# Kernel tuning notes

Measured on AMD Instinct MI355X. Metric: run time of the kernel, lower is better.

## Reference

```python
import jax, jax.numpy as jnp
import numpy as np

N_NODES = 50000
N_EDGES = 1600000
DIM_IN = 64
DIM = 64
DIM_OUT = 32
N_GRAPHS = 64
DELTA = 2.5749
BN_EPS = 1e-5


def _lin(x, W, b):
    return x @ W.T + b


def _pna_conv(x, src, dst, mlp_W, mlp_b, W1, b1, W2, b2):
    # GINConv with overridden PNA aggregate: nn(x + aggr(x_j))
    msgs = x[src]                                               # [E, d]
    n = x.shape[0]
    sums = jax.ops.segment_sum(msgs, dst, num_segments=n)       # [N, d]
    maxs = jax.ops.segment_max(msgs, dst, num_segments=n)
    cnt = jax.ops.segment_sum(jnp.ones((msgs.shape[0], 1), msgs.dtype), dst,
                              num_segments=n)                   # [N, 1]
    means = sums / cnt
    var = jax.nn.relu(jax.ops.segment_sum(msgs * msgs, dst, num_segments=n) / cnt
                      - means * means)
    aggr = jnp.concatenate([sums, maxs, means, var], axis=1)    # [N, 4d]
    comb = jnp.concatenate([aggr, (cnt / DELTA) * aggr, (DELTA / cnt) * aggr],
                           axis=1)                              # [N, 12d]
    a = _lin(comb, mlp_W, mlp_b)                                # [N, d]
    h = x + a                                                   # (1+eps)*x + aggr, eps=0
    return _lin(jax.nn.relu(_lin(h, W1, b1)), W2, b2)


def _bn(x, g, b):
    # BatchNorm1d with batch statistics (training-mode stats, biased var)
    m = x.mean(axis=0)
    v = ((x - m) ** 2).mean(axis=0)
    return g * (x - m) / jnp.sqrt(v + BN_EPS) + b


def setup_inputs() -> dict:
    key = jax.random.key(0)
    ks = jax.random.split(key, 32)
    x = jax.random.normal(ks[0], (N_NODES, DIM_IN), dtype=jnp.float32)
    src = jax.random.randint(ks[1], (N_EDGES,), 0, N_NODES)
    dst = jax.random.randint(ks[2], (N_EDGES,), 0, N_NODES)
    # guarantee every node has >=1 incoming edge (original divides by bincount)
    dst = dst.at[:N_NODES].set(jnp.arange(N_NODES))
    edge_index = jnp.stack([src, dst]).astype(jnp.int32)
    batch = jnp.sort(jax.random.randint(ks[3], (N_NODES,), 0, N_GRAPHS)).astype(jnp.int32)

    def w(k, shape):
        return jax.random.normal(k, shape, dtype=jnp.float32) * 0.1

    d = {"x": x, "edge_index": edge_index, "batch": batch}
    i = 4
    for c in ("c1", "c2", "c3"):
        d[f"{c}_mlp_W"] = w(ks[i], (DIM, DIM * 12)); i += 1
        d[f"{c}_mlp_b"] = jnp.zeros((DIM,), jnp.float32)
        d[f"{c}_W1"] = w(ks[i], (DIM, DIM)); i += 1
        d[f"{c}_b1"] = jnp.zeros((DIM,), jnp.float32)
        d[f"{c}_W2"] = w(ks[i], (DIM, DIM)); i += 1
        d[f"{c}_b2"] = jnp.zeros((DIM,), jnp.float32)
    for b in ("bn1", "bn2", "bn3"):
        d[f"{b}_g"] = jnp.ones((DIM,), jnp.float32)
        d[f"{b}_b"] = jnp.zeros((DIM,), jnp.float32)
    d["fc1_W"] = w(ks[i], (DIM, DIM)); i += 1
    d["fc1_b"] = jnp.zeros((DIM,), jnp.float32)
    d["fc2_W"] = w(ks[i], (DIM_OUT, DIM)); i += 1
    d["fc2_b"] = jnp.zeros((DIM_OUT,), jnp.float32)
    return d


def reference(x, edge_index, batch,
              c1_mlp_W, c1_mlp_b, c1_W1, c1_b1, c1_W2, c1_b2, bn1_g, bn1_b,
              c2_mlp_W, c2_mlp_b, c2_W1, c2_b1, c2_W2, c2_b2, bn2_g, bn2_b,
              c3_mlp_W, c3_mlp_b, c3_W1, c3_b1, c3_W2, c3_b2, bn3_g, bn3_b,
              fc1_W, fc1_b, fc2_W, fc2_b):
    src, dst = edge_index[0], edge_index[1]
    h = jax.nn.relu(_pna_conv(x, src, dst, c1_mlp_W, c1_mlp_b, c1_W1, c1_b1, c1_W2, c1_b2))
    h = _bn(h, bn1_g, bn1_b)
    h = jax.nn.relu(_pna_conv(h, src, dst, c2_mlp_W, c2_mlp_b, c2_W1, c2_b1, c2_W2, c2_b2))
    h = _bn(h, bn2_g, bn2_b)
    h = jax.nn.relu(_pna_conv(h, src, dst, c3_mlp_W, c3_mlp_b, c3_W1, c3_b1, c3_W2, c3_b2))
    h = _bn(h, bn3_g, bn3_b)
    g = jax.ops.segment_sum(h, batch, num_segments=N_GRAPHS)   # global_add_pool
    g = jax.nn.relu(_lin(g, fc1_W, fc1_b))                     # dropout disabled (eval)
    g = _lin(g, fc2_W, fc2_b)
    return jax.nn.log_softmax(g, axis=-1)
```

## Files before the change

kernel.cpp:

```cpp
#include <hip/hip_runtime.h>

#define NN 50000
#define NE 1600000
#define DD 64
#define NGRAPH 64
#define DOUT 32
#define DELTA_F 2.5749f
#define BN_EPS_F 1e-5f

typedef unsigned short ushort;
typedef __attribute__((ext_vector_type(8))) short short8;
typedef __attribute__((ext_vector_type(4))) float floatx4;

static __device__ __forceinline__ float blo(unsigned u) {
    return __uint_as_float(u << 16);
}
static __device__ __forceinline__ float bhi(unsigned u) {
    return __uint_as_float(u & 0xFFFF0000u);
}
static __device__ __forceinline__ float bu2f(ushort u) {
    return __uint_as_float(((unsigned)u) << 16);
}
static __device__ __forceinline__ ushort f2bu(float f) {
    unsigned u = __float_as_uint(f);
    unsigned r = (u + 0x7FFF + ((u >> 16) & 1)) >> 16;
    return (ushort)r;
}
static __device__ __forceinline__ unsigned pk(float a, float b) {
    return ((unsigned)f2bu(b) << 16) | (unsigned)f2bu(a);
}

__global__ void k_init(int* __restrict__ counts, float* __restrict__ bnstat,
                       float* __restrict__ gpool) {
    int i = blockIdx.x * 256 + threadIdx.x;
    if (i < NN) counts[i] = 0;
    if (i < 384) bnstat[i] = 0.f;
    if (i < NGRAPH * DD) gpool[i] = 0.f;
}

__global__ void k_rank(const int* __restrict__ dst, int* __restrict__ counts,
                       int* __restrict__ rank) {
    int e = blockIdx.x * 256 + threadIdx.x;
    if (e < NE) rank[e] = atomicAdd(&counts[dst[e]], 1);
}

__global__ void k_scan_a(const int* __restrict__ counts, int* __restrict__ blockSums) {
    __shared__ int red[256];
    int tid = threadIdx.x;
    int gid = blockIdx.x * 256 + tid;
    int v = (gid < NN) ? counts[gid] : 0;
    red[tid] = v;
    __syncthreads();
    for (int s = 128; s > 0; s >>= 1) {
        if (tid < s) red[tid] += red[tid + s];
        __syncthreads();
    }
    if (tid == 0) blockSums[blockIdx.x] = red[0];
}

__global__ void k_scan_b(const int* __restrict__ blockSums, int* __restrict__ blockBase) {
    __shared__ int sh[256];
    int tid = threadIdx.x;
    int v = (tid < 196) ? blockSums[tid] : 0;
    sh[tid] = v;
    __syncthreads();
    for (int off = 1; off < 256; off <<= 1) {
        int t = (tid >= off) ? sh[tid - off] : 0;
        __syncthreads();
        sh[tid] += t;
        __syncthreads();
    }
    blockBase[tid] = sh[tid] - v;
}

__global__ void k_scan_c(const int* __restrict__ counts, const int* __restrict__ blockBase,
                         int* __restrict__ row_ptr) {
    __shared__ int sh[256];
    int tid = threadIdx.x;
    int gid = blockIdx.x * 256 + tid;
    int v = (gid < NN) ? counts[gid] : 0;
    sh[tid] = v;
    __syncthreads();
    for (int off = 1; off < 256; off <<= 1) {
        int t = (tid >= off) ? sh[tid - off] : 0;
        __syncthreads();
        sh[tid] += t;
        __syncthreads();
    }
    int excl = blockBase[blockIdx.x] + sh[tid] - v;
    if (gid <= NN) row_ptr[gid] = excl;
}

__global__ void k_place(const int* __restrict__ src, const int* __restrict__ dst,
                        const int* __restrict__ rank, const int* __restrict__ row_ptr,
                        int* __restrict__ csr_src) {
    int e = blockIdx.x * 256 + threadIdx.x;
    if (e < NE) csr_src[row_ptr[dst[e]] + rank[e]] = src[e];
}

__global__ void k_wprep(const float* __restrict__ w0, const float* __restrict__ w1,
                        const float* __restrict__ w2,
                        const float* __restrict__ a0, const float* __restrict__ a1,
                        const float* __restrict__ a2, const float* __restrict__ a3,
                        const float* __restrict__ a4, const float* __restrict__ a5,
                        ushort* __restrict__ Wb, float* __restrict__ Wsm) {
    int i = blockIdx.x * 256 + threadIdx.x;
    if (i < 3 * 65536) {
        int layer = i / 65536, r = i % 65536;
        const float* w = (layer == 0) ? w0 : ((layer == 1) ? w1 : w2);
        int c = r / 16384, r2 = r % 16384;
        int kb = r2 >> 11, r3 = r2 & 2047;
        int t = r3 >> 9, r4 = r3 & 511;
        int l = r4 >> 3, j = r4 & 7;
        int k = kb * 32 + (l >> 4) * 8 + j;
        int o = t * 16 + (l & 15);
        int g = (c == 0) ? 0 : ((c == 3) ? 2 : 1);
        float wv = w[o * 768 + g * 256 + k];
        ushort h = f2bu(wv);
        Wb[i] = (c == 2) ? f2bu(wv - bu2f(h)) : h;
    } else if (i < 3 * 65536 + 6 * 4096) {
        int r2 = i - 3 * 65536;
        int l = r2 >> 12, r = r2 & 4095;
        const float* w = (l == 0) ? a0 : (l == 1) ? a1 : (l == 2) ? a2
                       : (l == 3) ? a3 : (l == 4) ? a4 : a5;
        int o = r >> 6, j = r & 63;
        Wsm[l * 4096 + j * 64 + o] = w[r];
    }
}

__global__ void k_x2h(const float* __restrict__ x, ushort* __restrict__ XH) {
    int i = blockIdx.x * 256 + threadIdx.x;
    if (i < NN * 16) {
        float4 v = *(const float4*)(x + (size_t)i * 4);
        ushort4 h;
        h.x = f2bu(v.x); h.y = f2bu(v.y); h.z = f2bu(v.z); h.w = f2bu(v.w);
        *(ushort4*)(XH + (size_t)i * 4) = h;
    }
}

#define MBIAS(i) aux[i]
#define B1V(i)   aux[64 + (i)]
#define B2V(i)   aux[128 + (i)]
#define DEGV(m)  aux[192 + (m)]

__global__ __launch_bounds__(256, 4) void k_fused(
    const ushort* __restrict__ XH,
    const int* __restrict__ row_ptr, const int* __restrict__ csr_src,
    const ushort* __restrict__ Wbh,
    const float* __restrict__ mlp_b,
    const float* __restrict__ W1t, const float* __restrict__ b1,
    const float* __restrict__ W2t, const float* __restrict__ b2,
    float* __restrict__ Y, float* __restrict__ bnstat) {
    __shared__ __align__(16) char smem[26624];
    ushort* const Agh = (ushort*)smem;
    ushort* const Agl = (ushort*)(smem + 12800);
    float* const aux = (float*)(smem + 25600);
    float* const hsf = (float*)smem;

    const int tid = threadIdx.x;
    const int node0 = blockIdx.x * 32;

    if (tid < 64) {
        MBIAS(tid) = mlp_b[tid];
        B1V(tid) = b1[tid];
        B2V(tid) = b2[tid];
    }

    {
        const int l8 = tid & 7;
        const int m = tid >> 3;
        const int node = node0 + m;
        const int f0 = l8 * 8;
        const ushort* Xp = XH + f0;

        float s[8], q[8], mx[8];
#pragma unroll
        for (int i = 0; i < 8; ++i) { s[i] = 0.f; q[i] = 0.f; mx[i] = -3.402823466e38f; }

        auto acc8 = [&](const uint4& rr) {
            float v0 = blo(rr.x), v1 = bhi(rr.x);
            float v2 = blo(rr.y), v3 = bhi(rr.y);
            float v4 = blo(rr.z), v5 = bhi(rr.z);
            float v6 = blo(rr.w), v7 = bhi(rr.w);
            s[0] += v0; q[0] = fmaf(v0, v0, q[0]); mx[0] = fmaxf(mx[0], v0);
            s[1] += v1; q[1] = fmaf(v1, v1, q[1]); mx[1] = fmaxf(mx[1], v1);
            s[2] += v2; q[2] = fmaf(v2, v2, q[2]); mx[2] = fmaxf(mx[2], v2);
            s[3] += v3; q[3] = fmaf(v3, v3, q[3]); mx[3] = fmaxf(mx[3], v3);
            s[4] += v4; q[4] = fmaf(v4, v4, q[4]); mx[4] = fmaxf(mx[4], v4);
            s[5] += v5; q[5] = fmaf(v5, v5, q[5]); mx[5] = fmaxf(mx[5], v5);
            s[6] += v6; q[6] = fmaf(v6, v6, q[6]); mx[6] = fmaxf(mx[6], v6);
            s[7] += v7; q[7] = fmaf(v7, v7, q[7]); mx[7] = fmaxf(mx[7], v7);
        };

        int beg = 0, end = 0;
        if (node < NN) { beg = row_ptr[node]; end = row_ptr[node + 1]; }
        const int deg = end - beg;
        const int nb = (deg + 3) >> 2;

        uint4 ra[4], rb[4];
        int ia[4];
        if (nb > 0) {
#pragma unroll
            for (int j = 0; j < 4; ++j) {
                int e = beg + j;
                ia[j] = csr_src[(e < end) ? e : end - 1];
            }
#pragma unroll
            for (int j = 0; j < 4; ++j)
                ra[j] = *(const uint4*)(Xp + (size_t)ia[j] * 64);
            if (nb > 1) {
#pragma unroll
                for (int j = 0; j < 4; ++j) {
                    int e = beg + 4 + j;
                    ia[j] = csr_src[(e < end) ? e : end - 1];
                }
            }
        }
        for (int t = 0; t < nb; ++t) {
            if (t + 1 < nb) {
#pragma unroll
                for (int j = 0; j < 4; ++j)
                    rb[j] = *(const uint4*)(Xp + (size_t)ia[j] * 64);
            }
            if (t + 2 < nb) {
                int b2e = beg + (t + 2) * 4;
#pragma unroll
                for (int j = 0; j < 4; ++j) {
                    int e = b2e + j;
                    ia[j] = csr_src[(e < end) ? e : end - 1];
                }
            }
            int cnt = end - (beg + t * 4);
            if (cnt >= 4) {
#pragma unroll
                for (int j = 0; j < 4; ++j) acc8(ra[j]);
            } else {
#pragma unroll
                for (int j = 0; j < 4; ++j) if (j < cnt) acc8(ra[j]);
            }
            if (t + 1 < nb) {
#pragma unroll
                for (int j = 0; j < 4; ++j) ra[j] = rb[j];
            }
        }

        float cdeg = (node < NN) ? (float)deg : 1.f;
        float rc = 1.0f / cdeg;
        float var[8];
#pragma unroll
        for (int i = 0; i < 8; ++i) {
            float mean = s[i] * rc;
            var[i] = fmaxf(q[i] * rc - mean * mean, 0.f);
            if (node >= NN) { mx[i] = 0.f; var[i] = 0.f; }
        }
        ushort* dh = Agh + m * 200 + f0;
        ushort* dl = Agl + m * 200 + f0;
        auto emit8 = [&](const float* v, int off) {
            ushort h0 = f2bu(v[0]), h1 = f2bu(v[1]), h2 = f2bu(v[2]), h3 = f2bu(v[3]);
            ushort h4 = f2bu(v[4]), h5 = f2bu(v[5]), h6 = f2bu(v[6]), h7 = f2bu(v[7]);
            uint4 hv;
            hv.x = (unsigned)h0 | ((unsigned)h1 << 16);
            hv.y = (unsigned)h2 | ((unsigned)h3 << 16);
            hv.z = (unsigned)h4 | ((unsigned)h5 << 16);
            hv.w = (unsigned)h6 | ((unsigned)h7 << 16);
            uint4 lv;
            lv.x = pk(v[0] - bu2f(h0), v[1] - bu2f(h1));
            lv.y = pk(v[2] - bu2f(h2), v[3] - bu2f(h3));
            lv.z = pk(v[4] - bu2f(h4), v[5] - bu2f(h5));
            lv.w = pk(v[6] - bu2f(h6), v[7] - bu2f(h7));
            *(uint4*)(dh + off) = hv;
            *(uint4*)(dl + off) = lv;
        };
        emit8(s, 0);
        emit8(mx, 64);
        emit8(var, 128);
        if (l8 == 0) DEGV(m) = cdeg;
    }
    __syncthreads();

    const int ln = tid & 63, wvi = tid >> 6;
    const int quad = ln >> 4, l16 = ln & 15;
    const int mtile = wvi >> 1;
    const int nt0 = (wvi & 1) * 2;

    const ushort* ArowH = Agh + (mtile * 16 + l16) * 200 + quad * 8;
    const ushort* ArowL = Agl + (mtile * 16 + l16) * 200 + quad * 8;
    short8 afh[6], afl[6];
#pragma unroll
    for (int i = 0; i < 6; ++i) {
        const int off = (i >> 1) * 64 + (i & 1) * 32;
        afh[i] = *(const short8*)(ArowH + off);
        afl[i] = *(const short8*)(ArowL + off);
    }
    __syncthreads();

#pragma unroll
    for (int nti = 0; nti < 2; ++nti) {
        const int nt = nt0 + nti;
        floatx4 aA0 = (floatx4){0.f, 0.f, 0.f, 0.f};
        floatx4 aB0 = (floatx4){0.f, 0.f, 0.f, 0.f};
        floatx4 aA1 = (floatx4){0.f, 0.f, 0.f, 0.f};
        floatx4 aB1 = (floatx4){0.f, 0.f, 0.f, 0.f};
        floatx4 aA2 = (floatx4){0.f, 0.f, 0.f, 0.f};
        floatx4 aB2 = (floatx4){0.f, 0.f, 0.f, 0.f};
#pragma unroll
        for (int kb = 0; kb < 8; ++kb) {
            const int am = (kb < 4) ? kb : ((kb < 6) ? (kb - 4) : (kb - 2));
            const int base = ((kb * 4 + nt) * 512) + ln * 8;
            short8 w0 = *(const short8*)(Wbh + base);
            short8 w1h = *(const short8*)(Wbh + 16384 + base);
            short8 w2 = *(const short8*)(Wbh + 3 * 16384 + base);
            if (kb == 4 || kb == 5) {
                aB0 = __builtin_amdgcn_mfma_f32_16x16x32_bf16(afh[am], w0, aB0, 0, 0, 0);
                aB1 = __builtin_amdgcn_mfma_f32_16x16x32_bf16(afh[am], w1h, aB1, 0, 0, 0);
                aB2 = __builtin_amdgcn_mfma_f32_16x16x32_bf16(afh[am], w2, aB2, 0, 0, 0);
            } else {
                short8 w1l = *(const short8*)(Wbh + 2 * 16384 + base);
                aA0 = __builtin_amdgcn_mfma_f32_16x16x32_bf16(afh[am], w0, aA0, 0, 0, 0);
                aA1 = __builtin_amdgcn_mfma_f32_16x16x32_bf16(afh[am], w1h, aA1, 0, 0, 0);
                aA1 = __builtin_amdgcn_mfma_f32_16x16x32_bf16(afl[am], w1h, aA1, 0, 0, 0);
                aA1 = __builtin_amdgcn_mfma_f32_16x16x32_bf16(afh[am], w1l, aA1, 0, 0, 0);
                aA2 = __builtin_amdgcn_mfma_f32_16x16x32_bf16(afh[am], w2, aA2, 0, 0, 0);
            }
        }
#pragma unroll
        for (int r = 0; r < 4; ++r) {
            int m = mtile * 16 + quad * 4 + r;
            float dg = DEGV(m), rcd = 1.f / dg;
            float cA2 = DELTA_F * rcd;
            float cB2 = DELTA_F * rcd * rcd;
            float cA1 = dg * (1.0f / DELTA_F);
            int n = nt * 16 + l16;
            hsf[n * 34 + m] = aA0[r] + rcd * aB0[r]
                            + cA2 * aA2[r] + cB2 * aB2[r]
                            + cA1 * aA1[r] + (1.0f / DELTA_F) * aB1[r];
        }
    }
    __syncthreads();

    const int tx = tid & 15, ty = tid >> 4;
    const int o0 = tx * 4, n0 = ty * 2;
#pragma unroll
    for (int ni = 0; ni < 2; ++ni) {
        int n = n0 + ni;
        int node = node0 + n;
        float xa4[4] = {0.f, 0.f, 0.f, 0.f};
        if (node < NN) {
            ushort4 hx = *(const ushort4*)(XH + (size_t)node * DD + o0);
            xa4[0] = bu2f(hx.x); xa4[1] = bu2f(hx.y);
            xa4[2] = bu2f(hx.z); xa4[3] = bu2f(hx.w);
        }
#pragma unroll
        for (int oi = 0; oi < 4; ++oi) {
            int idx = (o0 + oi) * 34 + n;
            hsf[idx] = hsf[idx] + xa4[oi] + MBIAS(o0 + oi);
        }
    }
    __syncthreads();

    const float2* const hs2 = (const float2*)hsf;
    float l1[8];
#pragma unroll
    for (int i = 0; i < 8; ++i) l1[i] = 0.f;
#pragma unroll 4
    for (int j = 0; j < 64; ++j) {
        float2 a = hs2[j * 17 + ty];
        const float4 wv4 = *(const float4*)(W1t + j * 64 + o0);
        l1[0] += a.x * wv4.x; l1[1] += a.x * wv4.y; l1[2] += a.x * wv4.z; l1[3] += a.x * wv4.w;
        l1[4] += a.y * wv4.x; l1[5] += a.y * wv4.y; l1[6] += a.y * wv4.z; l1[7] += a.y * wv4.w;
    }
    __syncthreads();
#pragma unroll
    for (int ni = 0; ni < 2; ++ni)
#pragma unroll
        for (int oi = 0; oi < 4; ++oi)
            hsf[(o0 + oi) * 34 + n0 + ni] = fmaxf(l1[ni * 4 + oi] + B1V(o0 + oi), 0.f);
    __syncthreads();

    float l2[8];
#pragma unroll
    for (int i = 0; i < 8; ++i) l2[i] = 0.f;
#pragma unroll 4
    for (int j = 0; j < 64; ++j) {
        float2 a = hs2[j * 17 + ty];
        const float4 wv4 = *(const float4*)(W2t + j * 64 + o0);
        l2[0] += a.x * wv4.x; l2[1] += a.x * wv4.y; l2[2] += a.x * wv4.z; l2[3] += a.x * wv4.w;
        l2[4] += a.y * wv4.x; l2[5] += a.y * wv4.y; l2[6] += a.y * wv4.z; l2[7] += a.y * wv4.w;
    }
    __syncthreads();
#pragma unroll
    for (int ni = 0; ni < 2; ++ni) {
        int node = node0 + n0 + ni;
        float4 yv;
        yv.x = fmaxf(l2[ni * 4 + 0] + B2V(o0 + 0), 0.f);
        yv.y = fmaxf(l2[ni * 4 + 1] + B2V(o0 + 1), 0.f);
        yv.z = fmaxf(l2[ni * 4 + 2] + B2V(o0 + 2), 0.f);
        yv.w = fmaxf(l2[ni * 4 + 3] + B2V(o0 + 3), 0.f);
        if (node < NN) *(float4*)(Y + (size_t)node * DD + o0) = yv;
        hsf[(o0 + 0) * 34 + n0 + ni] = yv.x;
        hsf[(o0 + 1) * 34 + n0 + ni] = yv.y;
        hsf[(o0 + 2) * 34 + n0 + ni] = yv.z;
        hsf[(o0 + 3) * 34 + n0 + ni] = yv.w;
    }
    __syncthreads();

    if (tid < 64) {
        float s = 0.f, sq = 0.f;
        int lim = NN - node0;
        if (lim > 32) lim = 32;
        for (int n = 0; n < lim; ++n) {
            float v = hsf[tid * 34 + n];
            s += v;
            sq += v * v;
        }
        atomicAdd(&bnstat[tid], s);
        atomicAdd(&bnstat[64 + tid], sq);
    }
}

__global__ __launch_bounds__(256) void k_bnapply(
    const float* __restrict__ Y, const float* __restrict__ bs,
    const float* __restrict__ g, const float* __restrict__ b,
    ushort* __restrict__ XH,
    const int* __restrict__ batch, float* __restrict__ gpool, int do_pool) {
    __shared__ float sc[64], shf[64], pool[512];
    int tid = threadIdx.x;
    if (tid < 64) {
        float mean = bs[tid] * (1.f / NN);
        float var = fmaxf(bs[64 + tid] * (1.f / NN) - mean * mean, 0.f);
        float inv = rsqrtf(var + BN_EPS_F);
        float s = g[tid] * inv;
        sc[tid] = s;
        shf[tid] = b[tid] - mean * s;
    }
    __syncthreads();
    int i = blockIdx.x * 256 + tid;
    int n = i >> 4, fq = (i & 15) * 4;
    float4 r = make_float4(0.f, 0.f, 0.f, 0.f);
    bool valid = i < NN * 16;
    if (valid) {
        float4 y = *(const float4*)(Y + (size_t)i * 4);
        r.x = y.x * sc[fq + 0] + shf[fq + 0];
        r.y = y.y * sc[fq + 1] + shf[fq + 1];
        r.z = y.z * sc[fq + 2] + shf[fq + 2];
        r.w = y.w * sc[fq + 3] + shf[fq + 3];
        ushort4 h;
        h.x = f2bu(r.x); h.y = f2bu(r.y); h.z = f2bu(r.z); h.w = f2bu(r.w);
        *(ushort4*)(XH + (size_t)i * 4) = h;
    }
    if (do_pool) {
        int nfirst = blockIdx.x * 16;
        int nlast = nfirst + 15;
        if (nlast >= NN) nlast = NN - 1;
        int gmin = batch[nfirst], gmax = batch[nlast];
        int span = gmax - gmin + 1;
        if (span <= 8) {
            for (int j = tid; j < span * 64; j += 256) pool[j] = 0.f;
            __syncthreads();
            if (valid) {
                int gb = batch[n] - gmin;
                atomicAdd(&pool[gb * 64 + fq + 0], r.x);
                atomicAdd(&pool[gb * 64 + fq + 1], r.y);
                atomicAdd(&pool[gb * 64 + fq + 2], r.z);
                atomicAdd(&pool[gb * 64 + fq + 3], r.w);
            }
            __syncthreads();
            for (int j = tid; j < span * 64; j += 256)
                atomicAdd(&gpool[(size_t)(gmin + (j >> 6)) * 64 + (j & 63)], pool[j]);
        } else {
            if (valid) {
                float* gp = gpool + (size_t)batch[n] * DD + fq;
                atomicAdd(gp + 0, r.x);
                atomicAdd(gp + 1, r.y);
                atomicAdd(gp + 2, r.z);
                atomicAdd(gp + 3, r.w);
            }
        }
    }
}

__global__ __launch_bounds__(256) void k_head(const float* __restrict__ gpool,
                                              const float* __restrict__ fc1W, const float* __restrict__ fc1b,
                                              const float* __restrict__ fc2W, const float* __restrict__ fc2b,
                                              float* __restrict__ out) {
    __shared__ float sh[12576];
    float* const gs = sh;
    float* const w1t = sh + 4096;
    float* const z1s = sh + 8256;
    float* const b1s = sh + 12416;
    float* const b2s = sh + 12480;
    float* const w2t = sh;
    float* const z2s = sh + 4096;

    int tid = threadIdx.x;
    for (int i = tid; i < 4096; i += 256) {
        gs[i] = gpool[i];
        int o = i >> 6, j = i & 63;
        w1t[j * 65 + o] = fc1W[i];
    }
    if (tid < 64) b1s[tid] = fc1b[tid];
    if (tid < 32) b2s[tid] = fc2b[tid];
    __syncthreads();
    {
        int tx = tid & 15, ty = tid >> 4, o0 = tx * 4, g0 = ty * 4;
        float acc[16];
#pragma unroll
        for (int i = 0; i < 16; ++i) acc[i] = 0.f;
        for (int j = 0; j < 64; ++j) {
            float w0 = w1t[j * 65 + o0 + 0], w1 = w1t[j * 65 + o0 + 1];
            float w2 = w1t[j * 65 + o0 + 2], w3 = w1t[j * 65 + o0 + 3];
#pragma unroll
            for (int gi = 0; gi < 4; ++gi) {
                float a = gs[(g0 + gi) * 64 + j];
                acc[gi * 4 + 0] += a * w0; acc[gi * 4 + 1] += a * w1;
                acc[gi * 4 + 2] += a * w2; acc[gi * 4 + 3] += a * w3;
            }
        }
        __syncthreads();
#pragma unroll
        for (int gi = 0; gi < 4; ++gi)
#pragma unroll
            for (int oi = 0; oi < 4; ++oi)
                z1s[(g0 + gi) * 65 + o0 + oi] = fmaxf(acc[gi * 4 + oi] + b1s[o0 + oi], 0.f);
    }
    for (int i = tid; i < 2048; i += 256) {
        int o = i >> 6, j = i & 63;
        w2t[j * 33 + o] = fc2W[i];
    }
    __syncthreads();
    {
        int tx = tid & 7, ty = tid >> 3, o0 = tx * 4, g0 = ty * 2;
        float acc[8];
#pragma unroll
        for (int i = 0; i < 8; ++i) acc[i] = 0.f;
        for (int j = 0; j < 64; ++j) {
            float w0 = w2t[j * 33 + o0 + 0], w1 = w2t[j * 33 + o0 + 1];
            float w2 = w2t[j * 33 + o0 + 2], w3 = w2t[j * 33 + o0 + 3];
            float a0 = z1s[(g0 + 0) * 65 + j];
            float a1 = z1s[(g0 + 1) * 65 + j];
            acc[0] += a0 * w0; acc[1] += a0 * w1; acc[2] += a0 * w2; acc[3] += a0 * w3;
            acc[4] += a1 * w0; acc[5] += a1 * w1; acc[6] += a1 * w2; acc[7] += a1 * w3;
        }
#pragma unroll
        for (int gi = 0; gi < 2; ++gi)
#pragma unroll
            for (int oi = 0; oi < 4; ++oi)
                z2s[(g0 + gi) * 33 + o0 + oi] = acc[gi * 4 + oi] + b2s[o0 + oi];
    }
    __syncthreads();
    if (tid < 64) {
        float m = -3.402823466e38f;
        for (int c = 0; c < DOUT; ++c) m = fmaxf(m, z2s[tid * 33 + c]);
        float s = 0.f;
        for (int c = 0; c < DOUT; ++c) s += expf(z2s[tid * 33 + c] - m);
        float lse = m + logf(s);
        for (int c = 0; c < DOUT; ++c)
            out[tid * DOUT + c] = z2s[tid * 33 + c] - lse;
    }
}

extern "C" void kernel_launch(void* const* d_in, const int* in_sizes, int n_in,
                              void* d_out, int out_size, void* d_ws, size_t ws_size,
                              hipStream_t stream) {
    const float* x = (const float*)d_in[0];
    const int* ei = (const int*)d_in[1];
    const int* src = ei;
    const int* dst = ei + NE;
    const int* batch = (const int*)d_in[2];
    const float *mlpW[3], *mlpB[3], *w1[3], *bb1[3], *w2[3], *bb2[3], *bng[3], *bnb[3];
    for (int l = 0; l < 3; ++l) {
        mlpW[l] = (const float*)d_in[3 + 6 * l];
        mlpB[l] = (const float*)d_in[4 + 6 * l];
        w1[l]   = (const float*)d_in[5 + 6 * l];
        bb1[l]  = (const float*)d_in[6 + 6 * l];
        w2[l]   = (const float*)d_in[7 + 6 * l];
        bb2[l]  = (const float*)d_in[8 + 6 * l];
        bng[l]  = (const float*)d_in[21 + 2 * l];
        bnb[l]  = (const float*)d_in[22 + 2 * l];
    }
    const float* fc1W = (const float*)d_in[27];
    const float* fc1b = (const float*)d_in[28];
    const float* fc2W = (const float*)d_in[29];
    const float* fc2b = (const float*)d_in[30];
    float* out = (float*)d_out;

    char* ws = (char*)d_ws;
    size_t off = 0;
    auto alloc = [&](size_t bytes) -> void* {
        void* p = ws + off;
        off = (off + bytes + 511) & ~(size_t)511;
        return p;
    };
    int* counts    = (int*)alloc((size_t)NN * 4);
    int* row_ptr   = (int*)alloc((size_t)(NN + 1) * 4);
    int* rank      = (int*)alloc((size_t)NE * 4);
    int* blockSums = (int*)alloc(256 * 4);
    int* blockBase = (int*)alloc(256 * 4);
    int* csr_src   = (int*)alloc((size_t)NE * 4);
    float* Yb      = (float*)alloc((size_t)NN * DD * 4);
    ushort* XH     = (ushort*)alloc((size_t)NN * DD * 2);
    ushort* Wb     = (ushort*)alloc((size_t)3 * 65536 * 2);
    float* Wsm     = (float*)alloc((size_t)6 * 4096 * 4);
    float* bnstat  = (float*)alloc(384 * 4);
    float* gpool   = (float*)alloc((size_t)NGRAPH * DD * 4);
    (void)ws_size; (void)in_sizes; (void)n_in; (void)out_size;

    k_init<<<196, 256, 0, stream>>>(counts, bnstat, gpool);
    k_rank<<<6250, 256, 0, stream>>>(dst, counts, rank);
    k_scan_a<<<196, 256, 0, stream>>>(counts, blockSums);
    k_scan_b<<<1, 256, 0, stream>>>(blockSums, blockBase);
    k_scan_c<<<196, 256, 0, stream>>>(counts, blockBase, row_ptr);
    k_place<<<6250, 256, 0, stream>>>(src, dst, rank, row_ptr, csr_src);
    k_wprep<<<864, 256, 0, stream>>>(mlpW[0], mlpW[1], mlpW[2],
                                     w1[0], w2[0], w1[1], w2[1], w1[2], w2[2],
                                     Wb, Wsm);
    k_x2h<<<3125, 256, 0, stream>>>(x, XH);

    for (int l = 0; l < 3; ++l) {
        k_fused<<<1563, 256, 0, stream>>>(XH, row_ptr, csr_src,
                                          Wb + (size_t)l * 65536,
                                          mlpB[l],
                                          Wsm + (size_t)(2 * l) * 4096, bb1[l],
                                          Wsm + (size_t)(2 * l + 1) * 4096, bb2[l],
                                          Yb, bnstat + l * 128);
        k_bnapply<<<3125, 256, 0, stream>>>(Yb, bnstat + l * 128, bng[l], bnb[l],
                                            XH, batch, gpool, (l == 2) ? 1 : 0);
    }
    k_head<<<1, 256, 0, stream>>>(gpool, fc1W, fc1b, fc2W, fc2b, out);
}
```

Measured before the change: 523.9 us.

## Fold BatchNorm affine into next layer's aggregation and merge prep kernels

The per-layer BN-apply kernels are removed. Each layer now writes the pre-BN ReLU output straight to bf16, and the next fused kernel applies the BN affine algebraically to the aggregated sum, max, variance and the self term. The init, weight-prep and x-to-bf16 kernels are merged into one prep kernel, and only the final layer keeps an fp32 output for pooling. This cuts several launches and a full read/write pass over node features per layer. The cost is that BN is applied after bf16 rounding of the pre-BN values, which slightly changes numerics, and the max rewrite is only valid when the BN scale is non-negative.

```diff
diff --git a/kernel.cpp b/kernel.cpp
--- a/kernel.cpp
+++ b/kernel.cpp
@@ -30,81 +30,25 @@
     return ((unsigned)f2bu(b) << 16) | (unsigned)f2bu(a);
 }
 
-__global__ void k_init(int* __restrict__ counts, float* __restrict__ bnstat,
+__global__ void k_prep(const float* __restrict__ x, ushort* __restrict__ XH,
+                       const float* __restrict__ w0, const float* __restrict__ w1,
+                       const float* __restrict__ w2,
+                       const float* __restrict__ a0, const float* __restrict__ a1,
+                       const float* __restrict__ a2, const float* __restrict__ a3,
+                       const float* __restrict__ a4, const float* __restrict__ a5,
+                       ushort* __restrict__ Wb, float* __restrict__ Wsm,
+                       int* __restrict__ counts, float* __restrict__ bnstat,
                        float* __restrict__ gpool) {
     int i = blockIdx.x * 256 + threadIdx.x;
     if (i < NN) counts[i] = 0;
     if (i < 384) bnstat[i] = 0.f;
     if (i < NGRAPH * DD) gpool[i] = 0.f;
-}
-
-__global__ void k_rank(const int* __restrict__ dst, int* __restrict__ counts,
-                       int* __restrict__ rank) {
-    int e = blockIdx.x * 256 + threadIdx.x;
-    if (e < NE) rank[e] = atomicAdd(&counts[dst[e]], 1);
-}
-
-__global__ void k_scan_a(const int* __restrict__ counts, int* __restrict__ blockSums) {
-    __shared__ int red[256];
-    int tid = threadIdx.x;
-    int gid = blockIdx.x * 256 + tid;
-    int v = (gid < NN) ? counts[gid] : 0;
-    red[tid] = v;
-    __syncthreads();
-    for (int s = 128; s > 0; s >>= 1) {
-        if (tid < s) red[tid] += red[tid + s];
-        __syncthreads();
-    }
-    if (tid == 0) blockSums[blockIdx.x] = red[0];
-}
-
-__global__ void k_scan_b(const int* __restrict__ blockSums, int* __restrict__ blockBase) {
-    __shared__ int sh[256];
-    int tid = threadIdx.x;
-    int v = (tid < 196) ? blockSums[tid] : 0;
-    sh[tid] = v;
-    __syncthreads();
-    for (int off = 1; off < 256; off <<= 1) {
-        int t = (tid >= off) ? sh[tid - off] : 0;
-        __syncthreads();
-        sh[tid] += t;
-        __syncthreads();
-    }
-    blockBase[tid] = sh[tid] - v;
-}
-
-__global__ void k_scan_c(const int* __restrict__ counts, const int* __restrict__ blockBase,
-                         int* __restrict__ row_ptr) {
-    __shared__ int sh[256];
-    int tid = threadIdx.x;
-    int gid = blockIdx.x * 256 + tid;
-    int v = (gid < NN) ? counts[gid] : 0;
-    sh[tid] = v;
-    __syncthreads();
-    for (int off = 1; off < 256; off <<= 1) {
-        int t = (tid >= off) ? sh[tid - off] : 0;
-        __syncthreads();
-        sh[tid] += t;
-        __syncthreads();
-    }
-    int excl = blockBase[blockIdx.x] + sh[tid] - v;
-    if (gid <= NN) row_ptr[gid] = excl;
-}
-
-__global__ void k_place(const int* __restrict__ src, const int* __restrict__ dst,
-                        const int* __restrict__ rank, const int* __restrict__ row_ptr,
-                        int* __restrict__ csr_src) {
-    int e = blockIdx.x * 256 + threadIdx.x;
-    if (e < NE) csr_src[row_ptr[dst[e]] + rank[e]] = src[e];
-}
-
-__global__ void k_wprep(const float* __restrict__ w0, const float* __restrict__ w1,
-                        const float* __restrict__ w2,
-                        const float* __restrict__ a0, const float* __restrict__ a1,
-                        const float* __restrict__ a2, const float* __restrict__ a3,
-                        const float* __restrict__ a4, const float* __restrict__ a5,
-                        ushort* __restrict__ Wb, float* __restrict__ Wsm) {
-    int i = blockIdx.x * 256 + threadIdx.x;
+    if (i < NN * 16) {
+        float4 v = *(const float4*)(x + (size_t)i * 4);
+        ushort4 h;
+        h.x = f2bu(v.x); h.y = f2bu(v.y); h.z = f2bu(v.z); h.w = f2bu(v.w);
+        *(ushort4*)(XH + (size_t)i * 4) = h;
+    }
     if (i < 3 * 65536) {
         int layer = i / 65536, r = i % 65536;
         const float* w = (layer == 0) ? w0 : ((layer == 1) ? w1 : w2);
@@ -128,30 +72,85 @@
     }
 }
 
-__global__ void k_x2h(const float* __restrict__ x, ushort* __restrict__ XH) {
-    int i = blockIdx.x * 256 + threadIdx.x;
-    if (i < NN * 16) {
-        float4 v = *(const float4*)(x + (size_t)i * 4);
-        ushort4 h;
-        h.x = f2bu(v.x); h.y = f2bu(v.y); h.z = f2bu(v.z); h.w = f2bu(v.w);
-        *(ushort4*)(XH + (size_t)i * 4) = h;
-    }
+__global__ void k_rank(const int* __restrict__ dst, int* __restrict__ counts,
+                       int* __restrict__ rank) {
+    int e = blockIdx.x * 256 + threadIdx.x;
+    if (e < NE) rank[e] = atomicAdd(&counts[dst[e]], 1);
+}
+
+__global__ void k_scan_a(const int* __restrict__ counts, int* __restrict__ blockSums) {
+    __shared__ int red[256];
+    int tid = threadIdx.x;
+    int gid = blockIdx.x * 256 + tid;
+    int v = (gid < NN) ? counts[gid] : 0;
+    red[tid] = v;
+    __syncthreads();
+    for (int s = 128; s > 0; s >>= 1) {
+        if (tid < s) red[tid] += red[tid + s];
+        __syncthreads();
+    }
+    if (tid == 0) blockSums[blockIdx.x] = red[0];
+}
+
+__global__ void k_scan_b(const int* __restrict__ blockSums, int* __restrict__ blockBase) {
+    __shared__ int sh[256];
+    int tid = threadIdx.x;
+    int v = (tid < 196) ? blockSums[tid] : 0;
+    sh[tid] = v;
+    __syncthreads();
+    for (int off = 1; off < 256; off <<= 1) {
+        int t = (tid >= off) ? sh[tid - off] : 0;
+        __syncthreads();
+        sh[tid] += t;
+        __syncthreads();
+    }
+    blockBase[tid] = sh[tid] - v;
+}
+
+__global__ void k_scan_c(const int* __restrict__ counts, const int* __restrict__ blockBase,
+                         int* __restrict__ row_ptr) {
+    __shared__ int sh[256];
+    int tid = threadIdx.x;
+    int gid = blockIdx.x * 256 + tid;
+    int v = (gid < NN) ? counts[gid] : 0;
+    sh[tid] = v;
+    __syncthreads();
+    for (int off = 1; off < 256; off <<= 1) {
+        int t = (tid >= off) ? sh[tid - off] : 0;
+        __syncthreads();
+        sh[tid] += t;
+        __syncthreads();
+    }
+    int excl = blockBase[blockIdx.x] + sh[tid] - v;
+    if (gid <= NN) row_ptr[gid] = excl;
+}
+
+__global__ void k_place(const int* __restrict__ src, const int* __restrict__ dst,
+                        const int* __restrict__ rank, const int* __restrict__ row_ptr,
+                        int* __restrict__ csr_src) {
+    int e = blockIdx.x * 256 + threadIdx.x;
+    if (e < NE) csr_src[row_ptr[dst[e]] + rank[e]] = src[e];
 }
 
 #define MBIAS(i) aux[i]
 #define B1V(i)   aux[64 + (i)]
 #define B2V(i)   aux[128 + (i)]
 #define DEGV(m)  aux[192 + (m)]
+#define AFFS(i)  aux[224 + (i)]
+#define AFFB(i)  aux[288 + (i)]
 
 __global__ __launch_bounds__(256, 4) void k_fused(
-    const ushort* __restrict__ XH,
+    const ushort* __restrict__ XHin, ushort* __restrict__ XHout,
+    float* __restrict__ Yf,
     const int* __restrict__ row_ptr, const int* __restrict__ csr_src,
     const ushort* __restrict__ Wbh,
     const float* __restrict__ mlp_b,
     const float* __restrict__ W1t, const float* __restrict__ b1,
     const float* __restrict__ W2t, const float* __restrict__ b2,
-    float* __restrict__ Y, float* __restrict__ bnstat) {
-    __shared__ __align__(16) char smem[26624];
+    const float* __restrict__ affstat, const float* __restrict__ affg,
+    const float* __restrict__ affb,
+    float* __restrict__ bnstat) {
+    __shared__ __align__(16) char smem[27008];
     ushort* const Agh = (ushort*)smem;
     ushort* const Agl = (ushort*)(smem + 12800);
     float* const aux = (float*)(smem + 25600);
@@ -164,14 +163,25 @@
         MBIAS(tid) = mlp_b[tid];
         B1V(tid) = b1[tid];
         B2V(tid) = b2[tid];
-    }
+        float A = 1.f, Bv = 0.f;
+        if (affstat) {
+            float mean = affstat[tid] * (1.f / NN);
+            float var = fmaxf(affstat[64 + tid] * (1.f / NN) - mean * mean, 0.f);
+            float inv = rsqrtf(var + BN_EPS_F);
+            A = affg[tid] * inv;
+            Bv = affb[tid] - mean * A;
+        }
+        AFFS(tid) = A;
+        AFFB(tid) = Bv;
+    }
+    __syncthreads();
 
     {
         const int l8 = tid & 7;
         const int m = tid >> 3;
         const int node = node0 + m;
         const int f0 = l8 * 8;
-        const ushort* Xp = XH + f0;
+        const ushort* Xp = XHin + f0;
 
         float s[8], q[8], mx[8];
 #pragma unroll
@@ -252,6 +262,13 @@
             float mean = s[i] * rc;
             var[i] = fmaxf(q[i] * rc - mean * mean, 0.f);
             if (node >= NN) { mx[i] = 0.f; var[i] = 0.f; }
+        }
+#pragma unroll
+        for (int i = 0; i < 8; ++i) {
+            float Af = AFFS(f0 + i), Bf = AFFB(f0 + i);
+            s[i] = Af * s[i] + cdeg * Bf;
+            mx[i] = Af * mx[i] + Bf;
+            var[i] = Af * Af * var[i];
         }
         ushort* dh = Agh + m * 200 + f0;
         ushort* dl = Agl + m * 200 + f0;
@@ -346,9 +363,11 @@
         int node = node0 + n;
         float xa4[4] = {0.f, 0.f, 0.f, 0.f};
         if (node < NN) {
-            ushort4 hx = *(const ushort4*)(XH + (size_t)node * DD + o0);
-            xa4[0] = bu2f(hx.x); xa4[1] = bu2f(hx.y);
-            xa4[2] = bu2f(hx.z); xa4[3] = bu2f(hx.w);
+            ushort4 hx = *(const ushort4*)(XHin + (size_t)node * DD + o0);
+            xa4[0] = AFFS(o0 + 0) * bu2f(hx.x) + AFFB(o0 + 0);
+            xa4[1] = AFFS(o0 + 1) * bu2f(hx.y) + AFFB(o0 + 1);
+            xa4[2] = AFFS(o0 + 2) * bu2f(hx.z) + AFFB(o0 + 2);
+            xa4[3] = AFFS(o0 + 3) * bu2f(hx.w) + AFFB(o0 + 3);
         }
 #pragma unroll
         for (int oi = 0; oi < 4; ++oi) {
@@ -396,7 +415,15 @@
         yv.y = fmaxf(l2[ni * 4 + 1] + B2V(o0 + 1), 0.f);
         yv.z = fmaxf(l2[ni * 4 + 2] + B2V(o0 + 2), 0.f);
         yv.w = fmaxf(l2[ni * 4 + 3] + B2V(o0 + 3), 0.f);
-        if (node < NN) *(float4*)(Y + (size_t)node * DD + o0) = yv;
+        if (node < NN) {
+            if (XHout) {
+                ushort4 h;
+                h.x = f2bu(yv.x); h.y = f2bu(yv.y);
+                h.z = f2bu(yv.z); h.w = f2bu(yv.w);
+                *(ushort4*)(XHout + (size_t)node * DD + o0) = h;
+            }
+            if (Yf) *(float4*)(Yf + (size_t)node * DD + o0) = yv;
+        }
         hsf[(o0 + 0) * 34 + n0 + ni] = yv.x;
         hsf[(o0 + 1) * 34 + n0 + ni] = yv.y;
         hsf[(o0 + 2) * 34 + n0 + ni] = yv.z;
@@ -418,11 +445,10 @@
     }
 }
 
-__global__ __launch_bounds__(256) void k_bnapply(
+__global__ __launch_bounds__(256) void k_pool(
     const float* __restrict__ Y, const float* __restrict__ bs,
     const float* __restrict__ g, const float* __restrict__ b,
-    ushort* __restrict__ XH,
-    const int* __restrict__ batch, float* __restrict__ gpool, int do_pool) {
+    const int* __restrict__ batch, float* __restrict__ gpool) {
     __shared__ float sc[64], shf[64], pool[512];
     int tid = threadIdx.x;
     if (tid < 64) {
@@ -444,37 +470,32 @@
         r.y = y.y * sc[fq + 1] + shf[fq + 1];
         r.z = y.z * sc[fq + 2] + shf[fq + 2];
         r.w = y.w * sc[fq + 3] + shf[fq + 3];
-        ushort4 h;
-        h.x = f2bu(r.x); h.y = f2bu(r.y); h.z = f2bu(r.z); h.w = f2bu(r.w);
-        *(ushort4*)(XH + (size_t)i * 4) = h;
-    }
-    if (do_pool) {
-        int nfirst = blockIdx.x * 16;
-        int nlast = nfirst + 15;
-        if (nlast >= NN) nlast = NN - 1;
-        int gmin = batch[nfirst], gmax = batch[nlast];
-        int span = gmax - gmin + 1;
-        if (span <= 8) {
-            for (int j = tid; j < span * 64; j += 256) pool[j] = 0.f;
-            __syncthreads();
-            if (valid) {
-                int gb = batch[n] - gmin;
-                atomicAdd(&pool[gb * 64 + fq + 0], r.x);
-                atomicAdd(&pool[gb * 64 + fq + 1], r.y);
-                atomicAdd(&pool[gb * 64 + fq + 2], r.z);
-                atomicAdd(&pool[gb * 64 + fq + 3], r.w);
-            }
-            __syncthreads();
-            for (int j = tid; j < span * 64; j += 256)
-                atomicAdd(&gpool[(size_t)(gmin + (j >> 6)) * 64 + (j & 63)], pool[j]);
-        } else {
-            if (valid) {
-                float* gp = gpool + (size_t)batch[n] * DD + fq;
-                atomicAdd(gp + 0, r.x);
-                atomicAdd(gp + 1, r.y);
-                atomicAdd(gp + 2, r.z);
-                atomicAdd(gp + 3, r.w);
-            }
+    }
+    int nfirst = blockIdx.x * 16;
+    int nlast = nfirst + 15;
+    if (nlast >= NN) nlast = NN - 1;
+    int gmin = batch[nfirst], gmax = batch[nlast];
+    int span = gmax - gmin + 1;
+    if (span <= 8) {
+        for (int j = tid; j < span * 64; j += 256) pool[j] = 0.f;
+        __syncthreads();
+        if (valid) {
+            int gb = batch[n] - gmin;
+            atomicAdd(&pool[gb * 64 + fq + 0], r.x);
+            atomicAdd(&pool[gb * 64 + fq + 1], r.y);
+            atomicAdd(&pool[gb * 64 + fq + 2], r.z);
+            atomicAdd(&pool[gb * 64 + fq + 3], r.w);
+        }
+        __syncthreads();
+        for (int j = tid; j < span * 64; j += 256)
+            atomicAdd(&gpool[(size_t)(gmin + (j >> 6)) * 64 + (j & 63)], pool[j]);
+    } else {
+        if (valid) {
+            float* gp = gpool + (size_t)batch[n] * DD + fq;
+            atomicAdd(gp + 0, r.x);
+            atomicAdd(gp + 1, r.y);
+            atomicAdd(gp + 2, r.z);
+            atomicAdd(gp + 3, r.w);
         }
     }
 }
@@ -598,33 +619,39 @@
     int* blockBase = (int*)alloc(256 * 4);
     int* csr_src   = (int*)alloc((size_t)NE * 4);
     float* Yb      = (float*)alloc((size_t)NN * DD * 4);
-    ushort* XH     = (ushort*)alloc((size_t)NN * DD * 2);
+    ushort* XHA    = (ushort*)alloc((size_t)NN * DD * 2);
+    ushort* XHB    = (ushort*)alloc((size_t)NN * DD * 2);
     ushort* Wb     = (ushort*)alloc((size_t)3 * 65536 * 2);
     float* Wsm     = (float*)alloc((size_t)6 * 4096 * 4);
     float* bnstat  = (float*)alloc(384 * 4);
     float* gpool   = (float*)alloc((size_t)NGRAPH * DD * 4);
     (void)ws_size; (void)in_sizes; (void)n_in; (void)out_size;
 
-    k_init<<<196, 256, 0, stream>>>(counts, bnstat, gpool);
+    k_prep<<<3125, 256, 0, stream>>>(x, XHA,
+                                     mlpW[0], mlpW[1], mlpW[2],
+                                     w1[0], w2[0], w1[1], w2[1], w1[2], w2[2],
+                                     Wb, Wsm, counts, bnstat, gpool);
     k_rank<<<6250, 256, 0, stream>>>(dst, counts, rank);
     k_scan_a<<<196, 256, 0, stream>>>(counts, blockSums);
     k_scan_b<<<1, 256, 0, stream>>>(blockSums, blockBase);
     k_scan_c<<<196, 256, 0, stream>>>(counts, blockBase, row_ptr);
     k_place<<<6250, 256, 0, stream>>>(src, dst, rank, row_ptr, csr_src);
-    k_wprep<<<864, 256, 0, stream>>>(mlpW[0], mlpW[1], mlpW[2],
-                                     w1[0], w2[0], w1[1], w2[1], w1[2], w2[2],
-                                     Wb, Wsm);
-    k_x2h<<<3125, 256, 0, stream>>>(x, XH);
-
-    for (int l = 0; l < 3; ++l) {
-        k_fused<<<1563, 256, 0, stream>>>(XH, row_ptr, csr_src,
-                                          Wb + (size_t)l * 65536,
-                                          mlpB[l],
-                                          Wsm + (size_t)(2 * l) * 4096, bb1[l],
-                                          Wsm + (size_t)(2 * l + 1) * 4096, bb2[l],
-                                          Yb, bnstat + l * 128);
-        k_bnapply<<<3125, 256, 0, stream>>>(Yb, bnstat + l * 128, bng[l], bnb[l],
-                                            XH, batch, gpool, (l == 2) ? 1 : 0);
-    }
+
+    k_fused<<<1563, 256, 0, stream>>>(XHA, XHB, nullptr, row_ptr, csr_src,
+                                      Wb, mlpB[0],
+                                      Wsm, bb1[0], Wsm + 4096, bb2[0],
+                                      nullptr, nullptr, nullptr,
+                                      bnstat);
+    k_fused<<<1563, 256, 0, stream>>>(XHB, XHA, nullptr, row_ptr, csr_src,
+                                      Wb + 65536, mlpB[1],
+                                      Wsm + 2 * 4096, bb1[1], Wsm + 3 * 4096, bb2[1],
+                                      bnstat, bng[0], bnb[0],
+                                      bnstat + 128);
+    k_fused<<<1563, 256, 0, stream>>>(XHA, nullptr, Yb, row_ptr, csr_src,
+                                      Wb + 2 * 65536, mlpB[2],
+                                      Wsm + 4 * 4096, bb1[2], Wsm + 5 * 4096, bb2[2],
+                                      bnstat + 128, bng[1], bnb[1],
+                                      bnstat + 256);
+    k_pool<<<3125, 256, 0, stream>>>(Yb, bnstat + 256, bng[2], bnb[2], batch, gpool);
     k_head<<<1, 256, 0, stream>>>(gpool, fc1W, fc1b, fc2W, fc2b, out);
 }
```

After: 498.8 us. 1.05x faster.
